# Kernel optimization log

Hardware: AMD Instinct MI355X
Metric: run time of the kernel (lower is better)

## Reference

```python
import jax, jax.numpy as jnp
import numpy as np

D_MODEL = 1024
NUM_HEADS = 16
D_K = D_MODEL // NUM_HEADS


def setup_inputs() -> dict:
    key = jax.random.key(0)
    ks = jax.random.split(key, 9)
    s = 1.0 / np.sqrt(D_MODEL)
    x = jax.random.normal(ks[0], (4, 2048, D_MODEL), dtype=jnp.float32)
    Wq = jax.random.uniform(ks[1], (D_MODEL, D_MODEL), jnp.float32, -s, s)
    bq = jax.random.uniform(ks[2], (D_MODEL,), jnp.float32, -s, s)
    Wk = jax.random.uniform(ks[3], (D_MODEL, D_MODEL), jnp.float32, -s, s)
    bk = jax.random.uniform(ks[4], (D_MODEL,), jnp.float32, -s, s)
    Wv = jax.random.uniform(ks[5], (D_MODEL, D_MODEL), jnp.float32, -s, s)
    bv = jax.random.uniform(ks[6], (D_MODEL,), jnp.float32, -s, s)
    Wo = jax.random.uniform(ks[7], (D_MODEL, D_MODEL), jnp.float32, -s, s)
    bo = jax.random.uniform(ks[8], (D_MODEL,), jnp.float32, -s, s)
    return {"x": x, "Wq": Wq, "bq": bq, "Wk": Wk, "bk": bk,
            "Wv": Wv, "bv": bv, "Wo": Wo, "bo": bo}


def reference(x, Wq, bq, Wk, bk, Wv, bv, Wo, bo):
    B, T, C = x.shape
    H, Dk = NUM_HEADS, D_K
    # linear projections (torch Linear: x @ W.T + b; here W stored as [in,out])
    q = (x @ Wq + bq).reshape(B, T, H, Dk).transpose(0, 2, 1, 3)  # [B,H,T,Dk]
    k = (x @ Wk + bk).reshape(B, T, H, Dk).transpose(0, 2, 1, 3)
    v = (x @ Wv + bv).reshape(B, T, H, Dk).transpose(0, 2, 1, 3)
    scores = jnp.einsum("bhtd,bhsd->bhts", q, k) / jnp.sqrt(jnp.float32(Dk))
    attn = jax.nn.softmax(scores, axis=-1)  # [B,H,T,T]
    context = jnp.einsum("bhts,bhsd->bhtd", attn, v)
    context = context.transpose(0, 2, 1, 3).reshape(B, T, C)
    return context @ Wo + bo
```

## Files before the change

### kernel.cpp

```cpp
#include <hip/hip_runtime.h>
#include <hip/hip_bf16.h>
#include <stdint.h>

typedef short bf16x8 __attribute__((ext_vector_type(8)));
typedef float f32x4  __attribute__((ext_vector_type(4)));

#define MFMA16(a, b, c) __builtin_amdgcn_mfma_f32_16x16x32_bf16((a), (b), (c), 0, 0, 0)

__device__ __forceinline__ unsigned short f2bf(float f) {
    union { float f; unsigned int u; } v; v.f = f;
    unsigned int u = v.u;
    u += 0x7fffu + ((u >> 16) & 1u);
    return (unsigned short)(u >> 16);
}

__device__ __forceinline__ float exp2f_fast(float x) {
#if __has_builtin(__builtin_amdgcn_exp2f)
    return __builtin_amdgcn_exp2f(x);
#else
    return exp2f(x);
#endif
}

__device__ __forceinline__ unsigned int pack_bf2(float a, float b) {
    return (unsigned int)f2bf(a) | ((unsigned int)f2bf(b) << 16);
}

__device__ __forceinline__ void g2lds16(const void* g, void* l) {
    __builtin_amdgcn_global_load_lds(
        (const __attribute__((address_space(1))) void*)g,
        (__attribute__((address_space(3))) void*)l, 16, 0, 0);
}


__global__ __launch_bounds__(256) void convert_x_kernel(
    const float4* __restrict__ src, ushort4* __restrict__ dst)
{
    int i = blockIdx.x * 256 + threadIdx.x;
    float4 v = src[i];
    ushort4 o;
    o.x = f2bf(v.x); o.y = f2bf(v.y); o.z = f2bf(v.z); o.w = f2bf(v.w);
    dst[i] = o;
}

__global__ __launch_bounds__(256) void transpose_w_kernel(
    const float* __restrict__ src, unsigned short* __restrict__ dst)
{
    __shared__ float tile[64][65];
    const int k0 = blockIdx.x * 64, n0 = blockIdx.y * 64;
    const int tx = threadIdx.x & 63, ty = threadIdx.x >> 6;
    #pragma unroll
    for (int i = 0; i < 64; i += 4)
        tile[ty + i][tx] = src[(size_t)(k0 + ty + i) * 1024 + n0 + tx];
    __syncthreads();
    #pragma unroll
    for (int i = 0; i < 64; i += 4)
        dst[(size_t)(n0 + ty + i) * 1024 + k0 + tx] = f2bf(tile[tx][ty + i]);
}


#define QSCALE 0.18033688011112042f

template <int MODE>
__global__ __launch_bounds__(256, 2) void gemm_bt(
    const unsigned short* __restrict__ A, const unsigned short* __restrict__ Bt,
    const float* __restrict__ b0, const float* __restrict__ b1, const float* __restrict__ b2,
    unsigned short* __restrict__ Qb, unsigned short* __restrict__ Kb,
    unsigned short* __restrict__ Vt, float* __restrict__ out)
{
    __shared__ alignas(16) unsigned short As[128 * 32];
    __shared__ alignas(16) unsigned short Bs[128 * 32];

    const int t = threadIdx.x;
    const int m0 = blockIdx.y * 128, n0 = blockIdx.x * 128;
    const int lane = t & 63, w = t >> 6, quad = lane >> 4, c16 = lane & 15;
    const int moff = (w >> 1) * 64, noff = (w & 1) * 64;

    f32x4 acc[4][4];
    #pragma unroll
    for (int i = 0; i < 4; ++i)
        #pragma unroll
        for (int j = 0; j < 4; ++j)
            acc[i][j] = (f32x4){0.f, 0.f, 0.f, 0.f};

    const unsigned short* Ag = A + (size_t)(m0 + (t >> 2)) * 1024 + (t & 3) * 8;
    const unsigned short* Bg = Bt + (size_t)(n0 + (t >> 2)) * 1024 + (t & 3) * 8;
    unsigned short* Asl = As + t * 8;
    unsigned short* Bsl = Bs + t * 8;

    for (int k0 = 0; k0 < 1024; k0 += 32) {
        g2lds16(Ag + k0,             Asl);
        g2lds16(Ag + 64 * 1024 + k0, Asl + 2048);
        g2lds16(Bg + k0,             Bsl);
        g2lds16(Bg + 64 * 1024 + k0, Bsl + 2048);
        __syncthreads();

        bf16x8 af[4], bfr[4];
        #pragma unroll
        for (int ms = 0; ms < 4; ++ms)
            af[ms] = *(const bf16x8*)(As + (moff + ms * 16 + c16) * 32 + quad * 8);
        #pragma unroll
        for (int ns = 0; ns < 4; ++ns)
            bfr[ns] = *(const bf16x8*)(Bs + (noff + ns * 16 + c16) * 32 + quad * 8);
        #pragma unroll
        for (int ms = 0; ms < 4; ++ms)
            #pragma unroll
            for (int ns = 0; ns < 4; ++ns)
                acc[ms][ns] = MFMA16(af[ms], bfr[ns], acc[ms][ns]);
        __syncthreads();
    }

    #pragma unroll
    for (int ns = 0; ns < 4; ++ns) {
        const int n = n0 + noff + ns * 16 + c16;
        if (MODE == 0) {
            const int mat = n >> 10, nn = n & 1023;
            const int h = nn >> 6, d = nn & 63;
            const float bias = (mat == 0) ? b0[nn] : ((mat == 1) ? b1[nn] : b2[nn]);
            #pragma unroll
            for (int ms = 0; ms < 4; ++ms) {
                const int mbase = m0 + moff + ms * 16 + quad * 4;
                const int b = mbase >> 11, tbase = mbase & 2047;
                const int bh = b * 16 + h;
                if (mat == 2) {
                    ushort4 pk;
                    pk.x = f2bf(acc[ms][ns][0] + bias);
                    pk.y = f2bf(acc[ms][ns][1] + bias);
                    pk.z = f2bf(acc[ms][ns][2] + bias);
                    pk.w = f2bf(acc[ms][ns][3] + bias);
                    *(ushort4*)(Vt + ((size_t)bh * 64 + d) * 2048 + tbase) = pk;
                } else {
                    #pragma unroll
                    for (int r = 0; r < 4; ++r) {
                        float v = acc[ms][ns][r] + bias;
                        if (mat == 0) v *= QSCALE;
                        unsigned short* dst = (mat == 0) ? Qb : Kb;
                        dst[((size_t)bh * 2048 + tbase + r) * 64 + d] = f2bf(v);
                    }
                }
            }
        } else {
            const float bias = b0[n];
            #pragma unroll
            for (int ms = 0; ms < 4; ++ms) {
                #pragma unroll
                for (int r = 0; r < 4; ++r) {
                    const int m = m0 + moff + ms * 16 + quad * 4 + r;
                    out[(size_t)m * 1024 + n] = acc[ms][ns][r] + bias;
                }
            }
        }
    }
}


__global__ __launch_bounds__(128, 2) void attn_kernel(
    const unsigned short* __restrict__ Qb, const unsigned short* __restrict__ Kb,
    const unsigned short* __restrict__ Vt, unsigned short* __restrict__ ctx)
{
    __shared__ alignas(16) unsigned short Ks[64 * 64];
    __shared__ alignas(16) unsigned short Vs[64 * 64];
    __shared__ alignas(16) unsigned short pl[2][64 * 64];

    const int t = threadIdx.x, w = t >> 6, lane = t & 63;
    const int quad = lane >> 4, c16 = lane & 15;
    const int bh = blockIdx.y;
    const int qbase = blockIdx.x * 128 + w * 64;

    bf16x8 qf[4][2];
    #pragma unroll
    for (int mt = 0; mt < 4; ++mt) {
        const unsigned short* Qp = Qb + ((size_t)bh * 2048 + qbase + mt * 16 + c16) * 64;
        qf[mt][0] = *(const bf16x8*)(Qp + quad * 8);
        qf[mt][1] = *(const bf16x8*)(Qp + 32 + quad * 8);
    }

    float l_r[4] = {0.f, 0.f, 0.f, 0.f};
    f32x4 O[4][4];
    #pragma unroll
    for (int mt = 0; mt < 4; ++mt)
        #pragma unroll
        for (int dc = 0; dc < 4; ++dc) O[mt][dc] = (f32x4){0.f, 0.f, 0.f, 0.f};

    const int sgrp = (t & 7) ^ ((t >> 3) & 7);
    const unsigned short* Kgl = Kb + (size_t)bh * 131072 + (size_t)(t >> 3) * 64 + sgrp * 8;
    const unsigned short* Vgl = Vt + (size_t)bh * 131072 + (size_t)(t >> 3) * 2048 + sgrp * 8;
    unsigned short* Ksl = Ks + t * 8;
    unsigned short* Vsl = Vs + t * 8;
    unsigned short* plw = pl[w];
    const f32x4 fzero = {0.f, 0.f, 0.f, 0.f};

    for (int s0 = 0; s0 < 2048; s0 += 64) {
        #pragma unroll
        for (int q = 0; q < 4; ++q) {
            g2lds16(Kgl + s0 * 64 + q * 1024,  Ksl + q * 1024);
            g2lds16(Vgl + s0 + q * 32768,      Vsl + q * 1024);
        }
        __syncthreads();

        #pragma unroll
        for (int ct = 0; ct < 4; ++ct) {
            const int key = ct * 16 + c16;
            const bf16x8 kf0 = *(const bf16x8*)(Ks + key * 64 + ((quad ^ (key & 7)) << 3));
            const bf16x8 kf1 = *(const bf16x8*)(Ks + key * 64 + (((4 + quad) ^ (key & 7)) << 3));
            #pragma unroll
            for (int mt = 0; mt < 4; ++mt) {
                f32x4 sa = MFMA16(kf0, qf[mt][0], fzero);
                sa = MFMA16(kf1, qf[mt][1], sa);
                const float p0 = exp2f_fast(sa[0]);
                const float p1 = exp2f_fast(sa[1]);
                const float p2 = exp2f_fast(sa[2]);
                const float p3 = exp2f_fast(sa[3]);
                l_r[mt] += (p0 + p1) + (p2 + p3);
                uint2 pk;
                pk.x = pack_bf2(p0, p1);
                pk.y = pack_bf2(p2, p3);
                const int row = mt * 16 + c16;
                const int grp = ct * 2 + (quad >> 1);
                *(uint2*)(plw + row * 64 + ((grp ^ (row & 7)) << 3) + (quad & 1) * 4) = pk;
            }
        }
        asm volatile("s_waitcnt lgkmcnt(0)" ::: "memory");

        #pragma unroll
        for (int kt = 0; kt < 2; ++kt) {
            bf16x8 pa[4];
            #pragma unroll
            for (int mt = 0; mt < 4; ++mt) {
                const int row = mt * 16 + c16;
                pa[mt] = *(const bf16x8*)(plw + row * 64 + (((kt * 4 + quad) ^ (row & 7)) << 3));
            }
            #pragma unroll
            for (int dc = 0; dc < 4; ++dc) {
                const int d = dc * 16 + c16;
                const bf16x8 vf = *(const bf16x8*)(Vs + d * 64 + (((kt * 4 + quad) ^ (d & 7)) << 3));
                #pragma unroll
                for (int mt = 0; mt < 4; ++mt)
                    O[mt][dc] = MFMA16(pa[mt], vf, O[mt][dc]);
            }
        }
        __syncthreads();
    }

    #pragma unroll
    for (int mt = 0; mt < 4; ++mt) {
        l_r[mt] += __shfl_xor(l_r[mt], 16);
        l_r[mt] += __shfl_xor(l_r[mt], 32);
    }

    const int b = bh >> 4, h = bh & 15;
    #pragma unroll
    for (int mt = 0; mt < 4; ++mt) {
        float inv[4];
        #pragma unroll
        for (int r = 0; r < 4; ++r)
            inv[r] = 1.0f / __shfl(l_r[mt], quad * 4 + r);
        #pragma unroll
        for (int dc = 0; dc < 4; ++dc)
            #pragma unroll
            for (int r = 0; r < 4; ++r) {
                const int row = qbase + mt * 16 + quad * 4 + r;
                ctx[((size_t)(b * 2048 + row)) * 1024 + h * 64 + dc * 16 + c16] =
                    f2bf(O[mt][dc][r] * inv[r]);
            }
    }
}


extern "C" void kernel_launch(void* const* d_in, const int* in_sizes, int n_in,
                              void* d_out, int out_size, void* d_ws, size_t ws_size,
                              hipStream_t stream)
{
    const float* x  = (const float*)d_in[0];
    const float* Wq = (const float*)d_in[1];
    const float* bq = (const float*)d_in[2];
    const float* Wk = (const float*)d_in[3];
    const float* bk = (const float*)d_in[4];
    const float* Wv = (const float*)d_in[5];
    const float* bv = (const float*)d_in[6];
    const float* Wo = (const float*)d_in[7];
    const float* bo = (const float*)d_in[8];
    float* out = (float*)d_out;

    char* ws = (char*)d_ws;
    unsigned short* xb    = (unsigned short*)(ws);
    unsigned short* Wqkvt = (unsigned short*)(ws + (16u << 20));
    unsigned short* Wot   = (unsigned short*)(ws + (22u << 20));
    unsigned short* Vt    = (unsigned short*)(ws + (24u << 20));
    unsigned short* Qb    = (unsigned short*)((char*)d_out);
    unsigned short* Kb    = (unsigned short*)((char*)d_out + (16u << 20));

    convert_x_kernel<<<8192, 256, 0, stream>>>((const float4*)x, (ushort4*)xb);
    dim3 tg(16, 16);
    transpose_w_kernel<<<tg, 256, 0, stream>>>(Wq, Wqkvt);
    transpose_w_kernel<<<tg, 256, 0, stream>>>(Wk, Wqkvt + (1u << 20));
    transpose_w_kernel<<<tg, 256, 0, stream>>>(Wv, Wqkvt + (2u << 20));
    transpose_w_kernel<<<tg, 256, 0, stream>>>(Wo, Wot);

    gemm_bt<0><<<dim3(24, 64), 256, 0, stream>>>(xb, Wqkvt, bq, bk, bv, Qb, Kb, Vt, nullptr);
    attn_kernel<<<dim3(16, 64), 128, 0, stream>>>(Qb, Kb, Vt, xb );
    gemm_bt<1><<<dim3(8, 64), 256, 0, stream>>>(xb, Wot, bo, nullptr, nullptr,
                                                nullptr, nullptr, nullptr, out);
}
```

Baseline: 308.6 us.

## Feed softmax probabilities to PV MFMA from registers instead of LDS

The attention kernel no longer stages the probability tile through per-wave shared memory. Each lane's four exp values from the QK MFMA are packed straight into the A operand of the PV MFMA, with the upper half of the operand zeroed and matching V slices read from LDS. This removes the P store, reload and lgkm wait, and frees the shared buffer. In exchange the number of PV MFMAs doubles, since half of each operand is padding. bf16 rounding of P is also replaced by truncation, which slightly lowers precision.

```diff
diff --git a/kernel.cpp b/kernel.cpp
--- a/kernel.cpp
+++ b/kernel.cpp
@@ -12,6 +12,10 @@
     unsigned int u = v.u;
     u += 0x7fffu + ((u >> 16) & 1u);
     return (unsigned short)(u >> 16);
+}
+
+__device__ __forceinline__ unsigned int trunc_pk(float a, float b) {
+    return (__float_as_uint(a) >> 16) | (__float_as_uint(b) & 0xffff0000u);
 }
 
 __device__ __forceinline__ float exp2f_fast(float x) {
@@ -20,10 +24,6 @@
 #else
     return exp2f(x);
 #endif
-}
-
-__device__ __forceinline__ unsigned int pack_bf2(float a, float b) {
-    return (unsigned int)f2bf(a) | ((unsigned int)f2bf(b) << 16);
 }
 
 __device__ __forceinline__ void g2lds16(const void* g, void* l) {
@@ -160,7 +160,6 @@
 {
     __shared__ alignas(16) unsigned short Ks[64 * 64];
     __shared__ alignas(16) unsigned short Vs[64 * 64];
-    __shared__ alignas(16) unsigned short pl[2][64 * 64];
 
     const int t = threadIdx.x, w = t >> 6, lane = t & 63;
     const int quad = lane >> 4, c16 = lane & 15;
@@ -187,7 +186,6 @@
     const unsigned short* Vgl = Vt + (size_t)bh * 131072 + (size_t)(t >> 3) * 2048 + sgrp * 8;
     unsigned short* Ksl = Ks + t * 8;
     unsigned short* Vsl = Vs + t * 8;
-    unsigned short* plw = pl[w];
     const f32x4 fzero = {0.f, 0.f, 0.f, 0.f};
 
     for (int s0 = 0; s0 < 2048; s0 += 64) {
@@ -203,6 +201,15 @@
             const int key = ct * 16 + c16;
             const bf16x8 kf0 = *(const bf16x8*)(Ks + key * 64 + ((quad ^ (key & 7)) << 3));
             const bf16x8 kf1 = *(const bf16x8*)(Ks + key * 64 + (((4 + quad) ^ (key & 7)) << 3));
+
+            uint2 vf[4];
+            const int g = ct * 2 + (quad >> 1);
+            #pragma unroll
+            for (int dc = 0; dc < 4; ++dc) {
+                const int d = dc * 16 + c16;
+                vf[dc] = *(const uint2*)(Vs + d * 64 + ((g ^ (d & 7)) << 3) + (quad & 1) * 4);
+            }
+
             #pragma unroll
             for (int mt = 0; mt < 4; ++mt) {
                 f32x4 sa = MFMA16(kf0, qf[mt][0], fzero);
@@ -212,31 +219,16 @@
                 const float p2 = exp2f_fast(sa[2]);
                 const float p3 = exp2f_fast(sa[3]);
                 l_r[mt] += (p0 + p1) + (p2 + p3);
-                uint2 pk;
-                pk.x = pack_bf2(p0, p1);
-                pk.y = pack_bf2(p2, p3);
-                const int row = mt * 16 + c16;
-                const int grp = ct * 2 + (quad >> 1);
-                *(uint2*)(plw + row * 64 + ((grp ^ (row & 7)) << 3) + (quad & 1) * 4) = pk;
-            }
-        }
-        asm volatile("s_waitcnt lgkmcnt(0)" ::: "memory");
-
-        #pragma unroll
-        for (int kt = 0; kt < 2; ++kt) {
-            bf16x8 pa[4];
-            #pragma unroll
-            for (int mt = 0; mt < 4; ++mt) {
-                const int row = mt * 16 + c16;
-                pa[mt] = *(const bf16x8*)(plw + row * 64 + (((kt * 4 + quad) ^ (row & 7)) << 3));
-            }
-            #pragma unroll
-            for (int dc = 0; dc < 4; ++dc) {
-                const int d = dc * 16 + c16;
-                const bf16x8 vf = *(const bf16x8*)(Vs + d * 64 + (((kt * 4 + quad) ^ (d & 7)) << 3));
+                union { bf16x8 v; unsigned int d[4]; } af;
+                af.d[0] = trunc_pk(p0, p1);
+                af.d[1] = trunc_pk(p2, p3);
+                af.d[2] = 0u; af.d[3] = 0u;
                 #pragma unroll
-                for (int mt = 0; mt < 4; ++mt)
-                    O[mt][dc] = MFMA16(pa[mt], vf, O[mt][dc]);
+                for (int dc = 0; dc < 4; ++dc) {
+                    union { bf16x8 v; uint2 u[2]; } bfv;
+                    bfv.u[0] = vf[dc]; bfv.u[1] = vf[dc];
+                    O[mt][dc] = MFMA16(af.v, bfv.v, O[mt][dc]);
+                }
             }
         }
         __syncthreads();
```

After: 303.0 us. About the same (-1.8%).
